# Kernel tuning notes

Hardware: AMD Instinct MI355X
Metric: run time of the kernel (lower is better)

## Reference

```python
import jax, jax.numpy as jnp
import numpy as np

B, TX, TZ, DX, DZ, DATT, DMID, H, DOUT = 8, 1024, 1024, 1024, 1024, 64, 64, 16, 1024


def setup_inputs() -> dict:
    key = jax.random.key(0)
    ks = jax.random.split(key, 10)
    s = 0.02
    return {
        "x": jax.random.normal(ks[0], (B, TX, DX), jnp.float32),
        "z": jax.random.normal(ks[1], (B, TZ, DZ), jnp.float32),
        "Wq": jax.random.normal(ks[2], (H, DX, DATT), jnp.float32) * s,
        "bq": jax.random.normal(ks[3], (H, DATT), jnp.float32) * s,
        "Wk": jax.random.normal(ks[4], (H, DZ, DATT), jnp.float32) * s,
        "bk": jax.random.normal(ks[5], (H, DATT), jnp.float32) * s,
        "Wv": jax.random.normal(ks[6], (H, DZ, DMID), jnp.float32) * s,
        "bv": jax.random.normal(ks[7], (H, DMID), jnp.float32) * s,
        "Wp": jax.random.normal(ks[8], (H * DMID, DOUT), jnp.float32) * s,
        "bp": jax.random.normal(ks[9], (DOUT,), jnp.float32) * s,
        "mask": jnp.tril(jnp.ones((TX, TZ), dtype=bool)),  # causal
    }


def reference(x, z, Wq, bq, Wk, bk, Wv, bv, Wp, bp, mask):
    # Per-head projections (heads batched via stacked weights). bhxe = batch, head, x-pos, feat
    Q = jnp.einsum('bxd,hde->bhxe', x, Wq) + bq[None, :, None, :]
    K = jnp.einsum('bzd,hde->bhze', z, Wk) + bk[None, :, None, :]
    V = jnp.einsum('bzd,hde->bhze', z, Wv) + bv[None, :, None, :]
    # Scores, mask (set ~mask to -inf), then scale by 1/sqrt(Datt) (as original: mask before scale)
    S = jnp.einsum('bhxe,bhze->bhxz', Q, K)
    S = jnp.where(mask[None, None, :, :], S, -jnp.inf) * (1.0 / jnp.sqrt(jnp.asarray(DATT, S.dtype)))
    A = jax.nn.softmax(S, axis=-1)
    y = jnp.einsum('bhxz,bhze->bhxe', A, V)          # [B, H, Tx, Dmid]
    y_concat = y.transpose(0, 2, 1, 3).reshape(B, TX, H * DMID)  # concat heads
    return y_concat @ Wp + bp
```

## Files before the change

### kernel.cpp

```cpp
#include <hip/hip_runtime.h>
#include <stdint.h>


typedef float    f32x4  __attribute__((ext_vector_type(4)));
typedef __bf16   bf16x8 __attribute__((ext_vector_type(8)));
typedef unsigned short u16x4 __attribute__((ext_vector_type(4)));
typedef unsigned short u16x8 __attribute__((ext_vector_type(8)));

#define MASKNEG (-3.0e38f)
#define QSCALE_F (0.125f * 1.4426950408889634f)

__device__ __forceinline__ unsigned short f2bf(float f) {
  unsigned int u = __float_as_uint(f);
  u += 0x7fffu + ((u >> 16) & 1u);
  return (unsigned short)(u >> 16);
}

__device__ __forceinline__ void gload16(const void* g, void* s) {
  const __attribute__((address_space(1))) unsigned int* gp =
      (const __attribute__((address_space(1))) unsigned int*)(uintptr_t)g;
  __attribute__((address_space(3))) unsigned int* lp =
      (__attribute__((address_space(3))) unsigned int*)(unsigned int)(uintptr_t)s;
  __builtin_amdgcn_global_load_lds(gp, lp, 16, 0, 0);
}

__device__ __forceinline__ f32x4 mfma16(bf16x8 a, bf16x8 b, f32x4 c) {
  return __builtin_amdgcn_mfma_f32_16x16x32_bf16(a, b, c, 0, 0, 0);
}


__global__ __launch_bounds__(256) void k_cvt2(const float* __restrict__ x,
                                              const float* __restrict__ z,
                                              unsigned short* __restrict__ out) {
  int i = blockIdx.x * 256 + threadIdx.x;
  const int stride = gridDim.x * 256;
  for (; i < 2097152; i += stride) {
    const float* in = (i < 1048576) ? (x + (size_t)i * 8) : (z + (size_t)(i - 1048576) * 8);
    const f32x4* p = (const f32x4*)in;
    f32x4 a = p[0], b = p[1];
    u16x8 o;
    o[0] = f2bf(a[0]); o[1] = f2bf(a[1]); o[2] = f2bf(a[2]); o[3] = f2bf(a[3]);
    o[4] = f2bf(b[0]); o[5] = f2bf(b[1]); o[6] = f2bf(b[2]); o[7] = f2bf(b[3]);
    *(u16x8*)(out + (size_t)i * 8) = o;
  }
}

__global__ __launch_bounds__(256) void k_pack(const float* __restrict__ Wq,
                                              const float* __restrict__ Wk,
                                              const float* __restrict__ Wv,
                                              const float* __restrict__ Wp,
                                              unsigned short* __restrict__ Oq,
                                              unsigned short* __restrict__ Ok,
                                              unsigned short* __restrict__ Ov,
                                              unsigned short* __restrict__ Op) {
  __shared__ float tile[64][65];
  const int t = threadIdx.x;
  const int zid = blockIdx.z;
  if (zid < 3) {
    const float* W = zid == 0 ? Wq : (zid == 1 ? Wk : Wv);
    unsigned short* O = zid == 0 ? Oq : (zid == 1 ? Ok : Ov);
    const int h = blockIdx.x, d0 = blockIdx.y * 64;
    const int ee = t & 63, r0 = t >> 6;
#pragma unroll
    for (int dd = r0; dd < 64; dd += 4)
      tile[dd][ee] = W[(h * 1024 + d0 + dd) * 64 + ee];
    __syncthreads();
    const int d = t & 63, e0 = t >> 6;
#pragma unroll
    for (int e = e0; e < 64; e += 4)
      O[(h * 64 + e) * 1024 + d0 + d] = f2bf(tile[d][e]);
  } else {
    const int k0 = blockIdx.x * 64, n0 = blockIdx.y * 64;
    const int nn = t & 63, r0 = t >> 6;
#pragma unroll
    for (int kk = r0; kk < 64; kk += 4)
      tile[kk][nn] = Wp[(k0 + kk) * 1024 + n0 + nn];
    __syncthreads();
    const int kk = t & 63, e0 = t >> 6;
#pragma unroll
    for (int n2 = e0; n2 < 64; n2 += 4)
      Op[(n0 + n2) * 1024 + k0 + kk] = f2bf(tile[kk][n2]);
  }
}

__device__ __forceinline__ void gemm_body(const unsigned short* __restrict__ A,
                                          const unsigned short* __restrict__ Bt,
                                          const float* __restrict__ bias,
                                          void* __restrict__ outp,
                                          int mode, float oscale,
                                          int brow, int bcol,
                                          unsigned short* As, unsigned short* Bs) {
  const int tid = threadIdx.x;
  const int l = tid & 63, w = tid >> 6;
  const int lrow = l & 15, lk = l >> 4;
  const int wr = (w >> 1) * 128, wc = (w & 1) * 64;

  const int arow = tid >> 2;
  const int asrc = ((tid & 3) ^ ((arow >> 1) & 3)) * 8;
  const unsigned short* ag0 = A + (size_t)(brow + arow) * 1024 + asrc;
  const unsigned short* bg0 = Bt + (size_t)(bcol + arow) * 1024 + asrc;

  int aoff[8], boff[4];
#pragma unroll
  for (int m = 0; m < 8; m++) {
    int row = wr + m * 16 + lrow;
    aoff[m] = row * 64 + ((lk ^ ((row >> 1) & 3)) << 4);
  }
#pragma unroll
  for (int n = 0; n < 4; n++) {
    int col = wc + n * 16 + lrow;
    boff[n] = col * 64 + ((lk ^ ((col >> 1) & 3)) << 4);
  }

  f32x4 acc[8][4];
#pragma unroll
  for (int n = 0; n < 4; n++) {
    float bv = bias[bcol + wc + n * 16 + lrow];
#pragma unroll
    for (int m = 0; m < 8; m++) acc[m][n] = (f32x4){bv, bv, bv, bv};
  }

#define STAGE_G(kt, slot)                                                  \
  {                                                                        \
    char* asb = (char*)As + (slot) * 16384 + w * 1024;                     \
    char* bsb = (char*)Bs + (slot) * 8192 + w * 1024;                      \
    gload16(ag0 + (kt) * 32,          asb);                                \
    gload16(ag0 + (kt) * 32 + 65536,  asb + 4096);                         \
    gload16(ag0 + (kt) * 32 + 131072, asb + 8192);                         \
    gload16(ag0 + (kt) * 32 + 196608, asb + 12288);                        \
    gload16(bg0 + (kt) * 32,          bsb);                                \
    gload16(bg0 + (kt) * 32 + 65536,  bsb + 4096);                         \
  }

  STAGE_G(0, 0)
  STAGE_G(1, 1)
  asm volatile("s_waitcnt vmcnt(6)" ::: "memory");
  __builtin_amdgcn_s_barrier();
  __builtin_amdgcn_sched_barrier(0);

  int s0 = 0, s2 = 2;
#pragma unroll 1
  for (int kt = 0; kt < 32; kt++) {
    if (kt < 30) STAGE_G(kt + 2, s2)
    const char* ab = (const char*)As + s0 * 16384;
    const char* bb = (const char*)Bs + s0 * 8192;
    bf16x8 bfr[4];
#pragma unroll
    for (int n = 0; n < 4; n++) bfr[n] = *(const bf16x8*)(bb + boff[n]);
#pragma unroll
    for (int m = 0; m < 8; m++) {
      bf16x8 af = *(const bf16x8*)(ab + aoff[m]);
#pragma unroll
      for (int n = 0; n < 4; n++)
        acc[m][n] = mfma16(af, bfr[n], acc[m][n]);
    }
    if (kt < 31) {
      if (kt < 30) {
        asm volatile("s_waitcnt vmcnt(6)" ::: "memory");
      } else {
        asm volatile("s_waitcnt vmcnt(0)" ::: "memory");
      }
      __builtin_amdgcn_s_barrier();
      __builtin_amdgcn_sched_barrier(0);
    }
    s0 = (s0 == 2) ? 0 : s0 + 1;
    s2 = (s2 == 2) ? 0 : s2 + 1;
  }
#undef STAGE_G

  if (mode == 0) {
    unsigned short* C = (unsigned short*)outp;
#pragma unroll
    for (int m = 0; m < 8; m++) {
      int r = brow + wr + m * 16 + 4 * lk;
#pragma unroll
      for (int n = 0; n < 4; n++) {
        int c = bcol + wc + n * 16 + lrow;
        unsigned short* p = C + ((r >> 10) * 16 + (c >> 6)) * 65536 + (r & 1023) * 64 + (c & 63);
#pragma unroll
        for (int j = 0; j < 4; j++) p[j * 64] = f2bf(acc[m][n][j] * oscale);
      }
    }
  } else if (mode == 2) {
    unsigned short* C = (unsigned short*)outp;
#pragma unroll
    for (int m = 0; m < 8; m++) {
      int r = brow + wr + m * 16 + 4 * lk;
#pragma unroll
      for (int n = 0; n < 4; n++) {
        int c = bcol + wc + n * 16 + lrow;
        u16x4 o;
#pragma unroll
        for (int j = 0; j < 4; j++) o[j] = f2bf(acc[m][n][j]);
        *(u16x4*)(C + ((r >> 10) * 16 + (c >> 6)) * 65536 + (c & 63) * 1024 + (r & 1023)) = o;
      }
    }
  } else {
    float* C = (float*)outp;
#pragma unroll
    for (int m = 0; m < 8; m++) {
      int r = brow + wr + m * 16 + 4 * lk;
#pragma unroll
      for (int n = 0; n < 4; n++) {
        int c = bcol + wc + n * 16 + lrow;
#pragma unroll
        for (int j = 0; j < 4; j++) C[(r + j) * 1024 + c] = acc[m][n][j];
      }
    }
  }
}

__global__ __launch_bounds__(256, 2) void k_gemm_qkv(const unsigned short* __restrict__ Xb,
                                                     const unsigned short* __restrict__ Zb,
                                                     const unsigned short* __restrict__ Wqkv,
                                                     const float* __restrict__ bq,
                                                     const float* __restrict__ bk,
                                                     const float* __restrict__ bv,
                                                     unsigned short* __restrict__ Qp,
                                                     unsigned short* __restrict__ Kp,
                                                     unsigned short* __restrict__ Vtp) {
  __shared__ unsigned short As[24576];
  __shared__ unsigned short Bs[12288];
  const int brow = blockIdx.x * 256;
  const int cg = blockIdx.y;
  const int seg = cg >> 3;
  const int bcol = (cg & 7) * 128;
  const unsigned short* A = (seg == 0) ? Xb : Zb;
  const unsigned short* Bt = Wqkv + (size_t)seg * 1048576;
  const float* bias = (seg == 0) ? bq : (seg == 1 ? bk : bv);
  void* outp = (seg == 0) ? (void*)Qp : (seg == 1 ? (void*)Kp : (void*)Vtp);
  const int mode = (seg == 2) ? 2 : 0;
  const float oscale = (seg == 0) ? QSCALE_F : 1.0f;
  gemm_body(A, Bt, bias, outp, mode, oscale, brow, bcol, As, Bs);
}

__global__ __launch_bounds__(256, 2) void k_gemm(const unsigned short* __restrict__ A,
                                                 const unsigned short* __restrict__ Bt,
                                                 const float* __restrict__ bias,
                                                 void* __restrict__ outp,
                                                 int mode, float oscale) {
  __shared__ unsigned short As[24576];
  __shared__ unsigned short Bs[12288];
  gemm_body(A, Bt, bias, outp, mode, oscale, blockIdx.x * 256, blockIdx.y * 128, As, Bs);
}

__global__ __launch_bounds__(256, 2) void k_attn(const unsigned short* __restrict__ Qh,
                                                 const unsigned short* __restrict__ Kh,
                                                 const unsigned short* __restrict__ Vth,
                                                 unsigned short* __restrict__ Y) {
  __shared__ unsigned short Ks[16384];
  __shared__ unsigned short Vs[16384];
  __shared__ unsigned short Ps[8192];

  const int tid = threadIdx.x, l = tid & 63, w = tid >> 6;
  const int lrow = l & 15, lk = l >> 4;
  const int bh = blockIdx.y;
  const int pp = blockIdx.x;

  const unsigned short* Qb = Qh + bh * 65536;
  const unsigned short* Kb = Kh + bh * 65536;
  const unsigned short* Vb = Vth + bh * 65536;

  bf16x8 ones;
#pragma unroll
  for (int j = 0; j < 8; j++) ones[j] = (__bf16)1.0f;

  const int krl = l >> 3;
  const int kgp = l & 7;
  const unsigned short* kgsrc = Kb + (w * 32 + krl) * 64 + ((kgp ^ krl) * 8);
  const int vrl = l >> 4;
  const int vgp = l & 15;
  const int vr0 = w * 16 + 0 * 4 + vrl;
  const int vr1 = w * 16 + 1 * 4 + vrl;
  const int vr2 = w * 16 + 2 * 4 + vrl;
  const int vr3 = w * 16 + 3 * 4 + vrl;
  const int voff0 = vr0 * 1024 + ((vgp ^ (vr0 & 15)) * 8);
  const int voff1 = vr1 * 1024 + ((vgp ^ (vr1 & 15)) * 8);
  const int voff2 = vr2 * 1024 + ((vgp ^ (vr2 & 15)) * 8);
  const int voff3 = vr3 * 1024 + ((vgp ^ (vr3 & 15)) * 8);

  char* pw = (char*)Ps + w * 4096;

  const int b = bh >> 4, h = bh & 15;

#pragma unroll 1
  for (int hp = 0; hp < 2; hp++) {
    const int qi = hp == 0 ? (7 - pp) : pp;
    const int qw = qi * 128 + w * 32;
    const int qmax = qw + 31;

    bf16x8 qf[2][2];
#pragma unroll
    for (int qn = 0; qn < 2; qn++) {
      const unsigned short* qp = Qb + (qw + qn * 16 + lrow) * 64 + lk * 8;
      qf[qn][0] = *(const bf16x8*)qp;
      qf[qn][1] = *(const bf16x8*)(qp + 32);
    }

    float mm[2];
    f32x4 lsum[2], yacc[2][4];
#pragma unroll
    for (int qn = 0; qn < 2; qn++) {
      mm[qn] = MASKNEG;
      lsum[qn] = (f32x4){0.f, 0.f, 0.f, 0.f};
#pragma unroll
      for (int ef = 0; ef < 4; ef++) yacc[qn][ef] = (f32x4){0.f, 0.f, 0.f, 0.f};
    }

    const int nt = qi + 1;

    {
      char* kb = (char*)Ks + w * 4096;
      char* vb2 = (char*)Vs + w * 4096;
      gload16(kgsrc + 0,    kb);
      gload16(kgsrc + 512,  kb + 1024);
      gload16(kgsrc + 1024, kb + 2048);
      gload16(kgsrc + 1536, kb + 3072);
      gload16(Vb + voff0, vb2);
      gload16(Vb + voff1, vb2 + 1024);
      gload16(Vb + voff2, vb2 + 2048);
      gload16(Vb + voff3, vb2 + 3072);
    }
    __syncthreads();

#pragma unroll 1
    for (int t = 0; t < nt; t++) {
      const int z0 = t * 128;
      const int cur = t & 1;
      if (t < nt - 1) {
        const int zn = (t + 1) * 128;
        char* kb = (char*)Ks + (cur ^ 1) * 16384 + w * 4096;
        char* vb2 = (char*)Vs + (cur ^ 1) * 16384 + w * 4096;
        const unsigned short* kgt = kgsrc + zn * 64;
        gload16(kgt + 0,    kb);
        gload16(kgt + 512,  kb + 1024);
        gload16(kgt + 1024, kb + 2048);
        gload16(kgt + 1536, kb + 3072);
        gload16(Vb + voff0 + zn, vb2);
        gload16(Vb + voff1 + zn, vb2 + 1024);
        gload16(Vb + voff2 + zn, vb2 + 2048);
        gload16(Vb + voff3 + zn, vb2 + 3072);
      }

      if (z0 <= qmax) {
        const char* kbase = (const char*)Ks + cur * 16384;
        const char* vbase = (const char*)Vs + cur * 16384;

        f32x4 s[2][8];
#pragma unroll
        for (int qn = 0; qn < 2; qn++)
#pragma unroll
          for (int zf = 0; zf < 8; zf++) s[qn][zf] = (f32x4){0.f, 0.f, 0.f, 0.f};
#pragma unroll
        for (int zf = 0; zf < 8; zf++) {
          int zr = zf * 16 + lrow;
#pragma unroll
          for (int kf = 0; kf < 2; kf++) {
            bf16x8 kfr = *(const bf16x8*)(kbase + zr * 128 + (((kf * 4 + lk) ^ (zr & 7)) << 4));
            s[0][zf] = mfma16(kfr, qf[0][kf], s[0][zf]);
            s[1][zf] = mfma16(kfr, qf[1][kf], s[1][zf]);
          }
        }

        if (z0 + 127 > qw) {
#pragma unroll
          for (int qn = 0; qn < 2; qn++) {
            int qg = qw + qn * 16 + lrow;
#pragma unroll
            for (int zf = 0; zf < 8; zf++) {
              int zb = z0 + zf * 16 + 4 * lk;
#pragma unroll
              for (int j = 0; j < 4; j++)
                if (zb + j > qg) s[qn][zf][j] = MASKNEG;
            }
          }
        }

#pragma unroll
        for (int qn = 0; qn < 2; qn++) {
          f32x4 r4 = s[qn][0];
#pragma unroll
          for (int zf = 1; zf < 8; zf++)
#pragma unroll
            for (int j = 0; j < 4; j++) r4[j] = fmaxf(r4[j], s[qn][zf][j]);
          float rm = fmaxf(fmaxf(r4[0], r4[1]), fmaxf(r4[2], r4[3]));
          rm = fmaxf(rm, __shfl_xor(rm, 16));
          rm = fmaxf(rm, __shfl_xor(rm, 32));

          if (__any(rm > mm[qn] + 8.f)) {
            float mn = fmaxf(mm[qn], rm);
            float a = __builtin_amdgcn_exp2f(mm[qn] - mn);
            mm[qn] = mn;
            f32x4 av;
#pragma unroll
            for (int j = 0; j < 4; j++)
              av[j] = __shfl(a, (l & 48) | (lk * 4 + j));
            lsum[qn] *= av;
#pragma unroll
            for (int ef = 0; ef < 4; ef++) yacc[qn][ef] *= av;
          }
          float mk = mm[qn];
#pragma unroll
          for (int zf = 0; zf < 8; zf++)
#pragma unroll
            for (int j = 0; j < 4; j++)
              s[qn][zf][j] = __builtin_amdgcn_exp2f(s[qn][zf][j] - mk);
        }

#pragma unroll
        for (int hf = 0; hf < 2; hf++) {
          if (z0 + hf * 64 <= qmax) {
#pragma unroll
            for (int qn = 0; qn < 2; qn++) {
              int q = qn * 16 + lrow;
              char* rowp = pw + q * 128;
#pragma unroll
              for (int zf2 = 0; zf2 < 4; zf2++) {
                int zfg = hf * 4 + zf2;
                u16x4 o;
#pragma unroll
                for (int j = 0; j < 4; j++) o[j] = f2bf(s[qn][zfg][j]);
                int g = zf2 * 2 + (lk >> 1);
                *(u16x4*)(rowp + ((g ^ (q & 7)) << 4) + (lk & 1) * 8) = o;
              }
            }

            asm volatile("s_waitcnt lgkmcnt(0)" ::: "memory");
            __builtin_amdgcn_sched_barrier(0);

            bf16x8 pf[2][2];
#pragma unroll
            for (int qn = 0; qn < 2; qn++)
#pragma unroll
              for (int kf = 0; kf < 2; kf++)
                pf[qn][kf] = *(const bf16x8*)(pw + (qn * 16 + lrow) * 128 + (((kf * 4 + lk) ^ (lrow & 7)) << 4));

#pragma unroll
            for (int qn = 0; qn < 2; qn++)
#pragma unroll
              for (int kf = 0; kf < 2; kf++)
                lsum[qn] = mfma16(pf[qn][kf], ones, lsum[qn]);

#pragma unroll
            for (int ef = 0; ef < 4; ef++) {
              int er = ef * 16 + lrow;
#pragma unroll
              for (int kf = 0; kf < 2; kf++) {
                int g = hf * 8 + kf * 4 + lk;
                bf16x8 vf = *(const bf16x8*)(vbase + er * 256 + ((g ^ (er & 15)) << 4));
                yacc[0][ef] = mfma16(pf[0][kf], vf, yacc[0][ef]);
                yacc[1][ef] = mfma16(pf[1][kf], vf, yacc[1][ef]);
              }
            }
          }
        }
      }

      __syncthreads();
    }

#pragma unroll
    for (int qn = 0; qn < 2; qn++) {
      f32x4 rinv;
#pragma unroll
      for (int j = 0; j < 4; j++) rinv[j] = 1.0f / lsum[qn][j];
#pragma unroll
      for (int ef = 0; ef < 4; ef++) {
        int col = h * 64 + ef * 16 + lrow;
#pragma unroll
        for (int j = 0; j < 4; j++) {
          int x = qw + qn * 16 + lk * 4 + j;
          Y[(b * 1024 + x) * 1024 + col] = f2bf(yacc[qn][ef][j] * rinv[j]);
        }
      }
    }
  }
}

extern "C" void kernel_launch(void* const* d_in, const int* in_sizes, int n_in,
                              void* d_out, int out_size, void* d_ws, size_t ws_size,
                              hipStream_t stream) {
  const float* x  = (const float*)d_in[0];
  const float* z  = (const float*)d_in[1];
  const float* Wq = (const float*)d_in[2];
  const float* bq = (const float*)d_in[3];
  const float* Wk = (const float*)d_in[4];
  const float* bk = (const float*)d_in[5];
  const float* Wv = (const float*)d_in[6];
  const float* bv = (const float*)d_in[7];
  const float* Wp = (const float*)d_in[8];
  const float* bp = (const float*)d_in[9];
  (void)in_sizes; (void)n_in; (void)out_size; (void)ws_size;

  char* ws = (char*)d_ws;
  unsigned short* Xb  = (unsigned short*)(ws + 0);
  unsigned short* Zb  = (unsigned short*)(ws + 16777216);
  unsigned short* Wqt = (unsigned short*)(ws + 33554432);
  unsigned short* Wkt = (unsigned short*)(ws + 35651584);
  unsigned short* Wvt = (unsigned short*)(ws + 37748736);
  unsigned short* Wpt = (unsigned short*)(ws + 39845888);
  unsigned short* Qp  = (unsigned short*)(ws + 41943040);
  unsigned short* Kp  = (unsigned short*)(ws + 58720256);
  unsigned short* Vtp = (unsigned short*)(ws + 75497472);

  k_cvt2<<<dim3(2048), dim3(256), 0, stream>>>(x, z, Xb);
  k_pack<<<dim3(16, 16, 4), dim3(256), 0, stream>>>(Wq, Wk, Wv, Wp, Wqt, Wkt, Wvt, Wpt);

  k_gemm_qkv<<<dim3(32, 24), dim3(256), 0, stream>>>(Xb, Zb, Wqt, bq, bk, bv, Qp, Kp, Vtp);

  k_attn<<<dim3(4, 128), dim3(256), 0, stream>>>(Qp, Kp, Vtp, Xb );

  k_gemm<<<dim3(32, 8), dim3(256), 0, stream>>>(Xb, Wpt, bp, d_out, 3, 1.0f);
}
```

Measured before the change: 151.8 us.

## Read K/V directly from global memory in attention, drop LDS staging and barriers

The attention kernel no longer stages K and V tiles in shared memory through double-buffered async global-to-LDS loads. Each wave now loads its K and V fragments straight from global memory (relying on L1/L2 caching), and the per-tile __syncthreads is gone, so waves proceed independently and skip tiles past their causal limit with continue. The grid is also transposed so that consecutive blocks cover different batch-heads rather than query pairs of the same head. Costs: the four waves of a block now each fetch the same K/V from cache, and the loads are not prefetched ahead of use, so latency may be exposed.

```diff
diff --git a/kernel.cpp b/kernel.cpp
--- a/kernel.cpp
+++ b/kernel.cpp
@@ -248,14 +248,12 @@
                                                  const unsigned short* __restrict__ Kh,
                                                  const unsigned short* __restrict__ Vth,
                                                  unsigned short* __restrict__ Y) {
-  __shared__ unsigned short Ks[16384];
-  __shared__ unsigned short Vs[16384];
   __shared__ unsigned short Ps[8192];
 
   const int tid = threadIdx.x, l = tid & 63, w = tid >> 6;
   const int lrow = l & 15, lk = l >> 4;
-  const int bh = blockIdx.y;
-  const int pp = blockIdx.x;
+  const int bh = blockIdx.x;
+  const int pp = blockIdx.y;
 
   const unsigned short* Qb = Qh + bh * 65536;
   const unsigned short* Kb = Kh + bh * 65536;
@@ -264,20 +262,6 @@
   bf16x8 ones;
 #pragma unroll
   for (int j = 0; j < 8; j++) ones[j] = (__bf16)1.0f;
-
-  const int krl = l >> 3;
-  const int kgp = l & 7;
-  const unsigned short* kgsrc = Kb + (w * 32 + krl) * 64 + ((kgp ^ krl) * 8);
-  const int vrl = l >> 4;
-  const int vgp = l & 15;
-  const int vr0 = w * 16 + 0 * 4 + vrl;
-  const int vr1 = w * 16 + 1 * 4 + vrl;
-  const int vr2 = w * 16 + 2 * 4 + vrl;
-  const int vr3 = w * 16 + 3 * 4 + vrl;
-  const int voff0 = vr0 * 1024 + ((vgp ^ (vr0 & 15)) * 8);
-  const int voff1 = vr1 * 1024 + ((vgp ^ (vr1 & 15)) * 8);
-  const int voff2 = vr2 * 1024 + ((vgp ^ (vr2 & 15)) * 8);
-  const int voff3 = vr3 * 1024 + ((vgp ^ (vr3 & 15)) * 8);
 
   char* pw = (char*)Ps + w * 4096;
 
@@ -309,154 +293,119 @@
 
     const int nt = qi + 1;
 
-    {
-      char* kb = (char*)Ks + w * 4096;
-      char* vb2 = (char*)Vs + w * 4096;
-      gload16(kgsrc + 0,    kb);
-      gload16(kgsrc + 512,  kb + 1024);
-      gload16(kgsrc + 1024, kb + 2048);
-      gload16(kgsrc + 1536, kb + 3072);
-      gload16(Vb + voff0, vb2);
-      gload16(Vb + voff1, vb2 + 1024);
-      gload16(Vb + voff2, vb2 + 2048);
-      gload16(Vb + voff3, vb2 + 3072);
-    }
-    __syncthreads();
-
 #pragma unroll 1
     for (int t = 0; t < nt; t++) {
       const int z0 = t * 128;
-      const int cur = t & 1;
-      if (t < nt - 1) {
-        const int zn = (t + 1) * 128;
-        char* kb = (char*)Ks + (cur ^ 1) * 16384 + w * 4096;
-        char* vb2 = (char*)Vs + (cur ^ 1) * 16384 + w * 4096;
-        const unsigned short* kgt = kgsrc + zn * 64;
-        gload16(kgt + 0,    kb);
-        gload16(kgt + 512,  kb + 1024);
-        gload16(kgt + 1024, kb + 2048);
-        gload16(kgt + 1536, kb + 3072);
-        gload16(Vb + voff0 + zn, vb2);
-        gload16(Vb + voff1 + zn, vb2 + 1024);
-        gload16(Vb + voff2 + zn, vb2 + 2048);
-        gload16(Vb + voff3 + zn, vb2 + 3072);
-      }
-
-      if (z0 <= qmax) {
-        const char* kbase = (const char*)Ks + cur * 16384;
-        const char* vbase = (const char*)Vs + cur * 16384;
-
-        f32x4 s[2][8];
-#pragma unroll
-        for (int qn = 0; qn < 2; qn++)
-#pragma unroll
-          for (int zf = 0; zf < 8; zf++) s[qn][zf] = (f32x4){0.f, 0.f, 0.f, 0.f};
-#pragma unroll
-        for (int zf = 0; zf < 8; zf++) {
-          int zr = zf * 16 + lrow;
-#pragma unroll
-          for (int kf = 0; kf < 2; kf++) {
-            bf16x8 kfr = *(const bf16x8*)(kbase + zr * 128 + (((kf * 4 + lk) ^ (zr & 7)) << 4));
-            s[0][zf] = mfma16(kfr, qf[0][kf], s[0][zf]);
-            s[1][zf] = mfma16(kfr, qf[1][kf], s[1][zf]);
+      if (z0 > qmax) continue;
+
+      f32x4 s[2][8];
+#pragma unroll
+      for (int qn = 0; qn < 2; qn++)
+#pragma unroll
+        for (int zf = 0; zf < 8; zf++) s[qn][zf] = (f32x4){0.f, 0.f, 0.f, 0.f};
+#pragma unroll
+      for (int zf = 0; zf < 8; zf++) {
+        const unsigned short* krow = Kb + (size_t)(z0 + zf * 16 + lrow) * 64 + lk * 8;
+#pragma unroll
+        for (int kf = 0; kf < 2; kf++) {
+          bf16x8 kfr = *(const bf16x8*)(krow + kf * 32);
+          s[0][zf] = mfma16(kfr, qf[0][kf], s[0][zf]);
+          s[1][zf] = mfma16(kfr, qf[1][kf], s[1][zf]);
+        }
+      }
+
+      if (z0 + 127 > qw) {
+#pragma unroll
+        for (int qn = 0; qn < 2; qn++) {
+          int qg = qw + qn * 16 + lrow;
+#pragma unroll
+          for (int zf = 0; zf < 8; zf++) {
+            int zb = z0 + zf * 16 + 4 * lk;
+#pragma unroll
+            for (int j = 0; j < 4; j++)
+              if (zb + j > qg) s[qn][zf][j] = MASKNEG;
           }
         }
-
-        if (z0 + 127 > qw) {
+      }
+
+#pragma unroll
+      for (int qn = 0; qn < 2; qn++) {
+        f32x4 r4 = s[qn][0];
+#pragma unroll
+        for (int zf = 1; zf < 8; zf++)
+#pragma unroll
+          for (int j = 0; j < 4; j++) r4[j] = fmaxf(r4[j], s[qn][zf][j]);
+        float rm = fmaxf(fmaxf(r4[0], r4[1]), fmaxf(r4[2], r4[3]));
+        rm = fmaxf(rm, __shfl_xor(rm, 16));
+        rm = fmaxf(rm, __shfl_xor(rm, 32));
+
+        if (__any(rm > mm[qn] + 8.f)) {
+          float mn = fmaxf(mm[qn], rm);
+          float a = __builtin_amdgcn_exp2f(mm[qn] - mn);
+          mm[qn] = mn;
+          f32x4 av;
+#pragma unroll
+          for (int j = 0; j < 4; j++)
+            av[j] = __shfl(a, (l & 48) | (lk * 4 + j));
+          lsum[qn] *= av;
+#pragma unroll
+          for (int ef = 0; ef < 4; ef++) yacc[qn][ef] *= av;
+        }
+        float mk = mm[qn];
+#pragma unroll
+        for (int zf = 0; zf < 8; zf++)
+#pragma unroll
+          for (int j = 0; j < 4; j++)
+            s[qn][zf][j] = __builtin_amdgcn_exp2f(s[qn][zf][j] - mk);
+      }
+
+#pragma unroll
+      for (int hf = 0; hf < 2; hf++) {
+        if (z0 + hf * 64 <= qmax) {
 #pragma unroll
           for (int qn = 0; qn < 2; qn++) {
-            int qg = qw + qn * 16 + lrow;
-#pragma unroll
-            for (int zf = 0; zf < 8; zf++) {
-              int zb = z0 + zf * 16 + 4 * lk;
-#pragma unroll
-              for (int j = 0; j < 4; j++)
-                if (zb + j > qg) s[qn][zf][j] = MASKNEG;
+            int q = qn * 16 + lrow;
+            char* rowp = pw + q * 128;
+#pragma unroll
+            for (int zf2 = 0; zf2 < 4; zf2++) {
+              int zfg = hf * 4 + zf2;
+              u16x4 o;
+#pragma unroll
+              for (int j = 0; j < 4; j++) o[j] = f2bf(s[qn][zfg][j]);
+              int g = zf2 * 2 + (lk >> 1);
+              *(u16x4*)(rowp + ((g ^ (q & 7)) << 4) + (lk & 1) * 8) = o;
+            }
+          }
+
+          asm volatile("s_waitcnt lgkmcnt(0)" ::: "memory");
+          __builtin_amdgcn_sched_barrier(0);
+
+          bf16x8 pf[2][2];
+#pragma unroll
+          for (int qn = 0; qn < 2; qn++)
+#pragma unroll
+            for (int kf = 0; kf < 2; kf++)
+              pf[qn][kf] = *(const bf16x8*)(pw + (qn * 16 + lrow) * 128 + (((kf * 4 + lk) ^ (lrow & 7)) << 4));
+
+#pragma unroll
+          for (int qn = 0; qn < 2; qn++)
+#pragma unroll
+            for (int kf = 0; kf < 2; kf++)
+              lsum[qn] = mfma16(pf[qn][kf], ones, lsum[qn]);
+
+#pragma unroll
+          for (int ef = 0; ef < 4; ef++) {
+            const unsigned short* vrow = Vb + (size_t)(ef * 16 + lrow) * 1024 + z0;
+#pragma unroll
+            for (int kf = 0; kf < 2; kf++) {
+              int g = hf * 8 + kf * 4 + lk;
+              bf16x8 vf = *(const bf16x8*)(vrow + g * 8);
+              yacc[0][ef] = mfma16(pf[0][kf], vf, yacc[0][ef]);
+              yacc[1][ef] = mfma16(pf[1][kf], vf, yacc[1][ef]);
             }
           }
         }
-
-#pragma unroll
-        for (int qn = 0; qn < 2; qn++) {
-          f32x4 r4 = s[qn][0];
-#pragma unroll
-          for (int zf = 1; zf < 8; zf++)
-#pragma unroll
-            for (int j = 0; j < 4; j++) r4[j] = fmaxf(r4[j], s[qn][zf][j]);
-          float rm = fmaxf(fmaxf(r4[0], r4[1]), fmaxf(r4[2], r4[3]));
-          rm = fmaxf(rm, __shfl_xor(rm, 16));
-          rm = fmaxf(rm, __shfl_xor(rm, 32));
-
-          if (__any(rm > mm[qn] + 8.f)) {
-            float mn = fmaxf(mm[qn], rm);
-            float a = __builtin_amdgcn_exp2f(mm[qn] - mn);
-            mm[qn] = mn;
-            f32x4 av;
-#pragma unroll
-            for (int j = 0; j < 4; j++)
-              av[j] = __shfl(a, (l & 48) | (lk * 4 + j));
-            lsum[qn] *= av;
-#pragma unroll
-            for (int ef = 0; ef < 4; ef++) yacc[qn][ef] *= av;
-          }
-          float mk = mm[qn];
-#pragma unroll
-          for (int zf = 0; zf < 8; zf++)
-#pragma unroll
-            for (int j = 0; j < 4; j++)
-              s[qn][zf][j] = __builtin_amdgcn_exp2f(s[qn][zf][j] - mk);
-        }
-
-#pragma unroll
-        for (int hf = 0; hf < 2; hf++) {
-          if (z0 + hf * 64 <= qmax) {
-#pragma unroll
-            for (int qn = 0; qn < 2; qn++) {
-              int q = qn * 16 + lrow;
-              char* rowp = pw + q * 128;
-#pragma unroll
-              for (int zf2 = 0; zf2 < 4; zf2++) {
-                int zfg = hf * 4 + zf2;
-                u16x4 o;
-#pragma unroll
-                for (int j = 0; j < 4; j++) o[j] = f2bf(s[qn][zfg][j]);
-                int g = zf2 * 2 + (lk >> 1);
-                *(u16x4*)(rowp + ((g ^ (q & 7)) << 4) + (lk & 1) * 8) = o;
-              }
-            }
-
-            asm volatile("s_waitcnt lgkmcnt(0)" ::: "memory");
-            __builtin_amdgcn_sched_barrier(0);
-
-            bf16x8 pf[2][2];
-#pragma unroll
-            for (int qn = 0; qn < 2; qn++)
-#pragma unroll
-              for (int kf = 0; kf < 2; kf++)
-                pf[qn][kf] = *(const bf16x8*)(pw + (qn * 16 + lrow) * 128 + (((kf * 4 + lk) ^ (lrow & 7)) << 4));
-
-#pragma unroll
-            for (int qn = 0; qn < 2; qn++)
-#pragma unroll
-              for (int kf = 0; kf < 2; kf++)
-                lsum[qn] = mfma16(pf[qn][kf], ones, lsum[qn]);
-
-#pragma unroll
-            for (int ef = 0; ef < 4; ef++) {
-              int er = ef * 16 + lrow;
-#pragma unroll
-              for (int kf = 0; kf < 2; kf++) {
-                int g = hf * 8 + kf * 4 + lk;
-                bf16x8 vf = *(const bf16x8*)(vbase + er * 256 + ((g ^ (er & 15)) << 4));
-                yacc[0][ef] = mfma16(pf[0][kf], vf, yacc[0][ef]);
-                yacc[1][ef] = mfma16(pf[1][kf], vf, yacc[1][ef]);
-              }
-            }
-          }
-        }
-      }
-
-      __syncthreads();
+      }
     }
 
 #pragma unroll
@@ -508,7 +457,7 @@
 
   k_gemm_qkv<<<dim3(32, 24), dim3(256), 0, stream>>>(Xb, Zb, Wqt, bq, bk, bv, Qp, Kp, Vtp);
 
-  k_attn<<<dim3(4, 128), dim3(256), 0, stream>>>(Qp, Kp, Vtp, Xb );
+  k_attn<<<dim3(128, 4), dim3(256), 0, stream>>>(Qp, Kp, Vtp, Xb );
 
   k_gemm<<<dim3(32, 8), dim3(256), 0, stream>>>(Xb, Wpt, bp, d_out, 3, 1.0f);
 }
```

Result: slower. 182.9 us (+20.5%).
